# Performance work log

Measured on AMD Instinct MI355X. Metric: run time of the kernel, lower is better.

## Reference

```python
import jax, jax.numpy as jnp
import numpy as np

N_NODES = 100000


def _graph_conv(x, W, b, src, dst, norm):
    # DGL GraphConv(norm='left'): scale source features by 1/out_degree,
    # aggregate (sum over incoming edges). in_feats > out_feats so weight
    # multiply happens before aggregation (mathematically equivalent either way).
    h = x @ W  # [N, out]
    msg = (h * norm[:, None])[src]  # gather per-edge messages [E, out]
    agg = jax.ops.segment_sum(msg, dst, num_segments=N_NODES)
    return agg + b


def setup_inputs() -> dict:
    key = jax.random.key(0)
    ks = jax.random.split(key, 10)
    in_f, hid_f, out_f = 256, 128, 64
    n_edges = 1_600_000
    feat = jax.random.normal(ks[0], (N_NODES, in_f), dtype=jnp.float32)
    src = jax.random.randint(ks[1], (n_edges,), 0, N_NODES, dtype=jnp.int32)
    dst = jax.random.randint(ks[2], (n_edges,), 0, N_NODES, dtype=jnp.int32)
    noise = jax.random.normal(ks[3], (N_NODES, out_f), dtype=jnp.float32)
    s1 = 1.0 / np.sqrt(in_f)
    s2 = 1.0 / np.sqrt(hid_f)
    W_shared = jax.random.uniform(ks[4], (in_f, hid_f), minval=-s1, maxval=s1, dtype=jnp.float32)
    b_shared = jnp.zeros((hid_f,), jnp.float32)
    W_mu = jax.random.uniform(ks[5], (hid_f, out_f), minval=-s2, maxval=s2, dtype=jnp.float32)
    b_mu = jnp.zeros((out_f,), jnp.float32)
    W_ls = jax.random.uniform(ks[6], (hid_f, out_f), minval=-s2, maxval=s2, dtype=jnp.float32)
    b_ls = jnp.zeros((out_f,), jnp.float32)
    return {"feat": feat, "W_shared": W_shared, "b_shared": b_shared,
            "W_mu": W_mu, "b_mu": b_mu, "W_ls": W_ls, "b_ls": b_ls,
            "noise": noise, "src": src, "dst": dst}


def reference(feat, W_shared, b_shared, W_mu, b_mu, W_ls, b_ls, noise, src, dst):
    # left-norm: 1 / out_degree (clamped to >= 1, as DGL does)
    deg_out = jax.ops.segment_sum(jnp.ones_like(src, jnp.float32), src,
                                  num_segments=N_NODES)
    norm = 1.0 / jnp.maximum(deg_out, 1.0)
    # shared first GraphConv with ReLU activation
    h = jax.nn.relu(_graph_conv(feat, W_shared, b_shared, src, dst, norm))
    # two heads (no activation)
    mu = _graph_conv(h, W_mu, b_mu, src, dst, norm)
    log_sigma = _graph_conv(h, W_ls, b_ls, src, dst, norm)
    # reparameterized sample
    return mu + noise * jnp.exp(log_sigma)
```

## Files before the change

### kernel.cpp

```cpp
#include <hip/hip_runtime.h>
#include <hip/hip_bf16.h>
#include <math.h>

typedef __attribute__((ext_vector_type(8))) short short8;
typedef __attribute__((ext_vector_type(4))) float f32x4;

__device__ __forceinline__ unsigned short f2bf(float f) {
    unsigned int u = __float_as_uint(f);
    u += 0x7FFF + ((u >> 16) & 1);
    return (unsigned short)(u >> 16);
}
__device__ __forceinline__ float b2f(unsigned short s) {
    return __uint_as_float(((unsigned int)s) << 16);
}
__device__ __forceinline__ unsigned int f2bf2(float a, float b) {
    __hip_bfloat162 h = __float22bfloat162_rn(make_float2(a, b));
    return *(unsigned int*)&h;
}
__device__ __forceinline__ void gl_lds16(const void* g, void* l) {
    __builtin_amdgcn_global_load_lds(
        (const __attribute__((address_space(1))) void*)g,
        (__attribute__((address_space(3))) void*)l, 16, 0, 0);
}

#define EB 8192
#define BSH 10
#define NBKT 128

__global__ __launch_bounds__(256)
void k1_hist(const int* __restrict__ src, const int* __restrict__ dst,
             int* __restrict__ bhist, int E) {
    __shared__ int hist[256];
    int t = threadIdx.x;
    hist[t] = 0;
    __syncthreads();
    int base = blockIdx.x * EB;
    int end = min(base + EB, E);
    for (int e = base + 4 * t; e < end; e += 1024) {
        if (e + 3 < end) {
            int4 d4 = *(const int4*)&dst[e];
            int4 s4 = *(const int4*)&src[e];
            atomicAdd(&hist[d4.x >> BSH], 1);
            atomicAdd(&hist[d4.y >> BSH], 1);
            atomicAdd(&hist[d4.z >> BSH], 1);
            atomicAdd(&hist[d4.w >> BSH], 1);
            atomicAdd(&hist[128 + (s4.x >> BSH)], 1);
            atomicAdd(&hist[128 + (s4.y >> BSH)], 1);
            atomicAdd(&hist[128 + (s4.z >> BSH)], 1);
            atomicAdd(&hist[128 + (s4.w >> BSH)], 1);
        } else {
            for (int q = e; q < end; ++q) {
                atomicAdd(&hist[dst[q] >> BSH], 1);
                atomicAdd(&hist[128 + (src[q] >> BSH)], 1);
            }
        }
    }
    __syncthreads();
    bhist[(size_t)blockIdx.x * 256 + t] = hist[t];
}

__global__ __launch_bounds__(256)
void kc1_totals(const int* __restrict__ bhist, int* __restrict__ totals, int PB) {
    int t = threadIdx.x;
    int slice = (PB + 7) / 8;
    int b0 = blockIdx.x * slice;
    int b1 = min(b0 + slice, PB);
    int s = 0;
    for (int blk = b0; blk < b1; ++blk) s += bhist[(size_t)blk * 256 + t];
    if (s) atomicAdd(&totals[t], s);
}

__global__ __launch_bounds__(256)
void kc2_scan2(const int* __restrict__ totals, int* __restrict__ bbase_d,
               int* __restrict__ bbase_s) {
    __shared__ int s[256];
    int t = threadIdx.x;
    int v = totals[t];
    s[t] = v;
    __syncthreads();
    for (int off = 1; off < 128; off <<= 1) {
        int u = ((t & 127) >= off) ? s[t - off] : 0;
        __syncthreads();
        s[t] += u;
        __syncthreads();
    }
    int excl = s[t] - v;
    if (t < 128) bbase_d[t] = excl;
    else bbase_s[t - 128] = excl;
}

__global__ __launch_bounds__(256)
void kc3_boff(const int* __restrict__ bhist, const int* __restrict__ bbase_d,
              const int* __restrict__ bbase_s, int* __restrict__ boffT, int PB) {
    __shared__ int sums[256];
    int b = blockIdx.x;
    int t = threadIdx.x;
    int v = (t < PB) ? bhist[(size_t)t * 256 + b] : 0;
    sums[t] = v;
    __syncthreads();
    for (int off = 1; off < 256; off <<= 1) {
        int u = (t >= off) ? sums[t - off] : 0;
        __syncthreads();
        sums[t] += u;
        __syncthreads();
    }
    int base = (b < 128) ? bbase_d[b] : bbase_s[b - 128];
    if (t < PB) boffT[(size_t)b * PB + t] = base + sums[t] - v;
}

__global__ __launch_bounds__(256)
void k2_scatter(const int* __restrict__ src, const int* __restrict__ dst,
                const int* __restrict__ boffT, int2* __restrict__ parr,
                int* __restrict__ sarr, int E, int PB) {
    __shared__ int cnt[256];
    int t = threadIdx.x;
    int blk = blockIdx.x;
    cnt[t] = boffT[(size_t)t * PB + blk];
    __syncthreads();
    int base = blk * EB;
    int end = min(base + EB, E);
    for (int e = base + 4 * t; e < end; e += 1024) {
        if (e + 3 < end) {
            int4 s4 = *(const int4*)&src[e];
            int4 d4 = *(const int4*)&dst[e];
            int p0 = atomicAdd(&cnt[d4.x >> BSH], 1); parr[p0] = make_int2(s4.x, d4.x);
            int p1 = atomicAdd(&cnt[d4.y >> BSH], 1); parr[p1] = make_int2(s4.y, d4.y);
            int p2 = atomicAdd(&cnt[d4.z >> BSH], 1); parr[p2] = make_int2(s4.z, d4.z);
            int p3 = atomicAdd(&cnt[d4.w >> BSH], 1); parr[p3] = make_int2(s4.w, d4.w);
            int q0 = atomicAdd(&cnt[128 + (s4.x >> BSH)], 1); sarr[q0] = s4.x;
            int q1 = atomicAdd(&cnt[128 + (s4.y >> BSH)], 1); sarr[q1] = s4.y;
            int q2 = atomicAdd(&cnt[128 + (s4.z >> BSH)], 1); sarr[q2] = s4.z;
            int q3 = atomicAdd(&cnt[128 + (s4.w >> BSH)], 1); sarr[q3] = s4.w;
        } else {
            for (int q = e; q < end; ++q) {
                int sv = src[q], dv = dst[q];
                int pd = atomicAdd(&cnt[dv >> BSH], 1);
                parr[pd] = make_int2(sv, dv);
                int ps = atomicAdd(&cnt[128 + (sv >> BSH)], 1);
                sarr[ps] = sv;
            }
        }
    }
}

__global__ __launch_bounds__(1024)
void k3_dst(const int2* __restrict__ parr, const int* __restrict__ totals,
            const int* __restrict__ bbase_d, int* __restrict__ row_off,
            int* __restrict__ col, int N, int E) {
    __shared__ int hist[1024], sc[1024];
    int b = blockIdx.x, t = threadIdx.x;
    if (b == 0 && t == 0) row_off[N] = E;
    int ne = totals[b];
    int ebase = bbase_d[b];
    hist[t] = 0;
    __syncthreads();
    for (int i = t; i < ne; i += 1024)
        atomicAdd(&hist[parr[ebase + i].y & 1023], 1);
    __syncthreads();
    int h = hist[t];
    sc[t] = h;
    __syncthreads();
    for (int off = 1; off < 1024; off <<= 1) {
        int u = (t >= off) ? sc[t - off] : 0;
        __syncthreads();
        sc[t] += u;
        __syncthreads();
    }
    int excl = sc[t] - h;
    int node = b * 1024 + t;
    if (node < N) row_off[node] = ebase + excl;
    hist[t] = ebase + excl;
    __syncthreads();
    for (int i = t; i < ne; i += 1024) {
        int2 pr = parr[ebase + i];
        int slot = atomicAdd(&hist[pr.y & 1023], 1);
        col[slot] = pr.x;
    }
}

__global__ __launch_bounds__(1024)
void k3_src(const int* __restrict__ sarr, const int* __restrict__ totals_s,
            const int* __restrict__ bbase_s, float* __restrict__ norm, int N) {
    __shared__ int hist[1024];
    int b = blockIdx.x, t = threadIdx.x;
    int ne = totals_s[b];
    int sb = bbase_s[b];
    hist[t] = 0;
    __syncthreads();
    for (int i = t; i < ne; i += 1024)
        atomicAdd(&hist[sarr[sb + i] & 1023], 1);
    __syncthreads();
    int node = b * 1024 + t;
    if (node < N) {
        int d = hist[t];
        norm[node] = 1.0f / (float)(d > 1 ? d : 1);
    }
}

__global__ __launch_bounds__(256)
void k_wprep(const float* __restrict__ Wsh, const float* __restrict__ Wmu,
             const float* __restrict__ Wls, unsigned short* __restrict__ W1T,
             unsigned short* __restrict__ W2T) {
    int b = blockIdx.x, t = threadIdx.x;
    if (b < 128) {
        W1T[(size_t)b * 256 + t] = f2bf(Wsh[(size_t)t * 128 + b]);
    } else {
        int n = b - 128;
        if (t < 128) {
            float v = (n < 64) ? Wmu[(size_t)t * 64 + n]
                               : Wls[(size_t)t * 64 + (n - 64)];
            W2T[(size_t)n * 128 + t] = f2bf(v);
        }
    }
}

__global__ __launch_bounds__(256)
void k_gemm1(const float* __restrict__ A, int M,
             const unsigned short* __restrict__ W1T,
             const float* __restrict__ norm, unsigned short* __restrict__ outb) {
    __shared__ char ldsA[64 * 1040];
    const int w = threadIdx.x >> 6;
    const int lane = threadIdx.x & 63;
    const int quad = lane >> 4;
    const int l16 = lane & 15;
    const int cl = w * 16 + l16;
    const int r0 = blockIdx.x * 64;

#pragma unroll
    for (int i = 0; i < 16; ++i) {
        int row = r0 + w * 16 + i;
        if (row >= M) row = M - 1;
        const char* g = (const char*)A + (size_t)row * 1024 + lane * 16;
        char* l = ldsA + (w * 16 + i) * 1040 + lane * 16;
        gl_lds16(g, l);
    }

    short8 bw[2][8];
#pragma unroll
    for (int hf = 0; hf < 2; ++hf) {
        const unsigned short* wp = W1T + (size_t)(hf * 64 + cl) * 256 + quad * 8;
#pragma unroll
        for (int ks = 0; ks < 8; ++ks)
            bw[hf][ks] = *(const short8*)(wp + ks * 32);
    }
    __syncthreads();

    f32x4 acc[4][2];
#pragma unroll
    for (int m = 0; m < 4; ++m) {
        acc[m][0] = (f32x4){0.f, 0.f, 0.f, 0.f};
        acc[m][1] = (f32x4){0.f, 0.f, 0.f, 0.f};
    }
#pragma unroll
    for (int ks = 0; ks < 8; ++ks) {
#pragma unroll
        for (int m = 0; m < 4; ++m) {
            const float* pr = (const float*)(ldsA + (m * 16 + l16) * 1040 +
                                             (ks * 32 + quad * 8) * 4);
            float4 x = *(const float4*)pr;
            float4 y = *(const float4*)(pr + 4);
            union { short8 v; unsigned int u[4]; } c;
            c.u[0] = f2bf2(x.x, x.y);
            c.u[1] = f2bf2(x.z, x.w);
            c.u[2] = f2bf2(y.x, y.y);
            c.u[3] = f2bf2(y.z, y.w);
            acc[m][0] = __builtin_amdgcn_mfma_f32_16x16x32_bf16(bw[0][ks], c.v, acc[m][0], 0, 0, 0);
            acc[m][1] = __builtin_amdgcn_mfma_f32_16x16x32_bf16(bw[1][ks], c.v, acc[m][1], 0, 0, 0);
        }
    }
    const int colbase = w * 16 + quad * 4;
#pragma unroll
    for (int m = 0; m < 4; ++m) {
        int row = r0 + m * 16 + l16;
        if (row < M) {
            float nm = norm[row];
            ushort4 o0, o1;
            o0.x = f2bf(acc[m][0][0] * nm); o0.y = f2bf(acc[m][0][1] * nm);
            o0.z = f2bf(acc[m][0][2] * nm); o0.w = f2bf(acc[m][0][3] * nm);
            o1.x = f2bf(acc[m][1][0] * nm); o1.y = f2bf(acc[m][1][1] * nm);
            o1.z = f2bf(acc[m][1][2] * nm); o1.w = f2bf(acc[m][1][3] * nm);
            *(ushort4*)&outb[(size_t)row * 128 + colbase] = o0;
            *(ushort4*)&outb[(size_t)row * 128 + 64 + colbase] = o1;
        }
    }
}

__global__ __launch_bounds__(256)
void k_gemm2(const unsigned short* __restrict__ A, int M,
             const unsigned short* __restrict__ W2T,
             const float* __restrict__ norm, unsigned short* __restrict__ outb) {
    __shared__ char ldsB[16 * 1040];
    const int w = threadIdx.x >> 6;
    const int lane = threadIdx.x & 63;
    const int quad = lane >> 4;
    const int l16 = lane & 15;
    const int cl = w * 16 + l16;
    const int r0 = blockIdx.x * 64;

#pragma unroll
    for (int i = 0; i < 4; ++i) {
        int c = w * 4 + i;
        int crow = r0 + c * 4;
        if (crow + 4 > M) crow = M - 4;
        const char* g = (const char*)A + (size_t)crow * 256 + lane * 16;
        char* l = ldsB + c * 1040 + lane * 16;
        gl_lds16(g, l);
    }

    short8 bw[2][4];
#pragma unroll
    for (int hf = 0; hf < 2; ++hf) {
        const unsigned short* wp = W2T + (size_t)(hf * 64 + cl) * 128 + quad * 8;
#pragma unroll
        for (int ks = 0; ks < 4; ++ks)
            bw[hf][ks] = *(const short8*)(wp + ks * 32);
    }
    __syncthreads();

    f32x4 acc[4][2];
#pragma unroll
    for (int m = 0; m < 4; ++m) {
        acc[m][0] = (f32x4){0.f, 0.f, 0.f, 0.f};
        acc[m][1] = (f32x4){0.f, 0.f, 0.f, 0.f};
    }
#pragma unroll
    for (int ks = 0; ks < 4; ++ks) {
#pragma unroll
        for (int m = 0; m < 4; ++m) {
            int row = m * 16 + l16;
            short8 af = *(const short8*)(ldsB + (row >> 2) * 1040 + (row & 3) * 256 +
                                         (ks * 32 + quad * 8) * 2);
            acc[m][0] = __builtin_amdgcn_mfma_f32_16x16x32_bf16(bw[0][ks], af, acc[m][0], 0, 0, 0);
            acc[m][1] = __builtin_amdgcn_mfma_f32_16x16x32_bf16(bw[1][ks], af, acc[m][1], 0, 0, 0);
        }
    }
    const int colbase = w * 16 + quad * 4;
#pragma unroll
    for (int m = 0; m < 4; ++m) {
        int row = r0 + m * 16 + l16;
        if (row < M) {
            float nm = norm[row];
            ushort4 o0, o1;
            o0.x = f2bf(acc[m][0][0] * nm); o0.y = f2bf(acc[m][0][1] * nm);
            o0.z = f2bf(acc[m][0][2] * nm); o0.w = f2bf(acc[m][0][3] * nm);
            o1.x = f2bf(acc[m][1][0] * nm); o1.y = f2bf(acc[m][1][1] * nm);
            o1.z = f2bf(acc[m][1][2] * nm); o1.w = f2bf(acc[m][1][3] * nm);
            *(ushort4*)&outb[(size_t)row * 128 + colbase] = o0;
            *(ushort4*)&outb[(size_t)row * 128 + 64 + colbase] = o1;
        }
    }
}

__global__ __launch_bounds__(256)
void k_spmm_relu(const int* __restrict__ row_off, const int* __restrict__ col,
                 const unsigned short* __restrict__ hxb, const float* __restrict__ bias,
                 unsigned short* __restrict__ hb, int N) {
    int g = (blockIdx.x * blockDim.x + threadIdx.x) >> 5;
    int l = threadIdx.x & 31;
    if (g >= N) return;
    int e0 = row_off[g], e1 = row_off[g + 1];
    const ushort4* base = (const ushort4*)hxb;
    float4 acc = make_float4(0.f, 0.f, 0.f, 0.f);
    int e = e0;
    for (; e + 7 < e1; e += 8) {
        ushort4 v0 = base[(size_t)col[e] * 32 + l];
        ushort4 v1 = base[(size_t)col[e + 1] * 32 + l];
        ushort4 v2 = base[(size_t)col[e + 2] * 32 + l];
        ushort4 v3 = base[(size_t)col[e + 3] * 32 + l];
        ushort4 v4 = base[(size_t)col[e + 4] * 32 + l];
        ushort4 v5 = base[(size_t)col[e + 5] * 32 + l];
        ushort4 v6 = base[(size_t)col[e + 6] * 32 + l];
        ushort4 v7 = base[(size_t)col[e + 7] * 32 + l];
        acc.x += ((b2f(v0.x) + b2f(v1.x)) + (b2f(v2.x) + b2f(v3.x))) +
                 ((b2f(v4.x) + b2f(v5.x)) + (b2f(v6.x) + b2f(v7.x)));
        acc.y += ((b2f(v0.y) + b2f(v1.y)) + (b2f(v2.y) + b2f(v3.y))) +
                 ((b2f(v4.y) + b2f(v5.y)) + (b2f(v6.y) + b2f(v7.y)));
        acc.z += ((b2f(v0.z) + b2f(v1.z)) + (b2f(v2.z) + b2f(v3.z))) +
                 ((b2f(v4.z) + b2f(v5.z)) + (b2f(v6.z) + b2f(v7.z)));
        acc.w += ((b2f(v0.w) + b2f(v1.w)) + (b2f(v2.w) + b2f(v3.w))) +
                 ((b2f(v4.w) + b2f(v5.w)) + (b2f(v6.w) + b2f(v7.w)));
    }
    for (; e + 1 < e1; e += 2) {
        ushort4 a = base[(size_t)col[e] * 32 + l];
        ushort4 b = base[(size_t)col[e + 1] * 32 + l];
        acc.x += b2f(a.x) + b2f(b.x);
        acc.y += b2f(a.y) + b2f(b.y);
        acc.z += b2f(a.z) + b2f(b.z);
        acc.w += b2f(a.w) + b2f(b.w);
    }
    if (e < e1) {
        ushort4 a = base[(size_t)col[e] * 32 + l];
        acc.x += b2f(a.x); acc.y += b2f(a.y); acc.z += b2f(a.z); acc.w += b2f(a.w);
    }
    float4 bi = ((const float4*)bias)[l];
    ushort4 r;
    r.x = f2bf(fmaxf(acc.x + bi.x, 0.f));
    r.y = f2bf(fmaxf(acc.y + bi.y, 0.f));
    r.z = f2bf(fmaxf(acc.z + bi.z, 0.f));
    r.w = f2bf(fmaxf(acc.w + bi.w, 0.f));
    ((ushort4*)hb)[(size_t)g * 32 + l] = r;
}

__global__ __launch_bounds__(256)
void k_spmm_out(const int* __restrict__ row_off, const int* __restrict__ col,
                const unsigned short* __restrict__ hcb, const float* __restrict__ bmu,
                const float* __restrict__ bls, const float* __restrict__ noise,
                float* __restrict__ out, int N) {
    int g = (blockIdx.x * blockDim.x + threadIdx.x) >> 5;
    int l = threadIdx.x & 31;
    if (g >= N) return;
    int e0 = row_off[g], e1 = row_off[g + 1];
    const ushort4* base = (const ushort4*)hcb;
    float4 acc = make_float4(0.f, 0.f, 0.f, 0.f);
    int e = e0;
    for (; e + 7 < e1; e += 8) {
        ushort4 v0 = base[(size_t)col[e] * 32 + l];
        ushort4 v1 = base[(size_t)col[e + 1] * 32 + l];
        ushort4 v2 = base[(size_t)col[e + 2] * 32 + l];
        ushort4 v3 = base[(size_t)col[e + 3] * 32 + l];
        ushort4 v4 = base[(size_t)col[e + 4] * 32 + l];
        ushort4 v5 = base[(size_t)col[e + 5] * 32 + l];
        ushort4 v6 = base[(size_t)col[e + 6] * 32 + l];
        ushort4 v7 = base[(size_t)col[e + 7] * 32 + l];
        acc.x += ((b2f(v0.x) + b2f(v1.x)) + (b2f(v2.x) + b2f(v3.x))) +
                 ((b2f(v4.x) + b2f(v5.x)) + (b2f(v6.x) + b2f(v7.x)));
        acc.y += ((b2f(v0.y) + b2f(v1.y)) + (b2f(v2.y) + b2f(v3.y))) +
                 ((b2f(v4.y) + b2f(v5.y)) + (b2f(v6.y) + b2f(v7.y)));
        acc.z += ((b2f(v0.z) + b2f(v1.z)) + (b2f(v2.z) + b2f(v3.z))) +
                 ((b2f(v4.z) + b2f(v5.z)) + (b2f(v6.z) + b2f(v7.z)));
        acc.w += ((b2f(v0.w) + b2f(v1.w)) + (b2f(v2.w) + b2f(v3.w))) +
                 ((b2f(v4.w) + b2f(v5.w)) + (b2f(v6.w) + b2f(v7.w)));
    }
    for (; e + 1 < e1; e += 2) {
        ushort4 a = base[(size_t)col[e] * 32 + l];
        ushort4 b = base[(size_t)col[e + 1] * 32 + l];
        acc.x += b2f(a.x) + b2f(b.x);
        acc.y += b2f(a.y) + b2f(b.y);
        acc.z += b2f(a.z) + b2f(b.z);
        acc.w += b2f(a.w) + b2f(b.w);
    }
    if (e < e1) {
        ushort4 a = base[(size_t)col[e] * 32 + l];
        acc.x += b2f(a.x); acc.y += b2f(a.y); acc.z += b2f(a.z); acc.w += b2f(a.w);
    }
    int lane64 = threadIdx.x & 63;
    int p = (lane64 + 16) & 63;
    float lx = __shfl(acc.x, p, 64);
    float ly = __shfl(acc.y, p, 64);
    float lz = __shfl(acc.z, p, 64);
    float lw = __shfl(acc.w, p, 64);
    if (l < 16) {
        float4 bm = ((const float4*)bmu)[l];
        float4 bl = ((const float4*)bls)[l];
        float4 nz = ((const float4*)noise)[(size_t)g * 16 + l];
        float4 o;
        o.x = (acc.x + bm.x) + nz.x * expf(lx + bl.x);
        o.y = (acc.y + bm.y) + nz.y * expf(ly + bl.y);
        o.z = (acc.z + bm.z) + nz.z * expf(lz + bl.z);
        o.w = (acc.w + bm.w) + nz.w * expf(lw + bl.w);
        ((float4*)out)[(size_t)g * 16 + l] = o;
    }
}

static inline char* align64(char* p) {
    return (char*)(((uintptr_t)p + 63) & ~(uintptr_t)63);
}

extern "C" void kernel_launch(void* const* d_in, const int* in_sizes, int n_in,
                              void* d_out, int out_size, void* d_ws, size_t ws_size,
                              hipStream_t stream) {
    const float* feat  = (const float*)d_in[0];
    const float* Wsh   = (const float*)d_in[1];
    const float* bsh   = (const float*)d_in[2];
    const float* Wmu   = (const float*)d_in[3];
    const float* bmu   = (const float*)d_in[4];
    const float* Wls   = (const float*)d_in[5];
    const float* bls   = (const float*)d_in[6];
    const float* noise = (const float*)d_in[7];
    const int*   src   = (const int*)d_in[8];
    const int*   dst   = (const int*)d_in[9];
    float* out = (float*)d_out;

    const int N = in_sizes[0] / 256;
    const int E = in_sizes[8];
    const int PB = (E + EB - 1) / EB;

    char* p = (char*)d_ws;
    float* norm   = (float*)p;                  p += (size_t)N * 4;         p = align64(p);
    int* row_off  = (int*)p;                    p += (size_t)(N + 4) * 4;   p = align64(p);
    int* totals   = (int*)p;                    p += 256 * 4;
    int* bbase_d  = (int*)p;                    p += 128 * 4;
    int* bbase_s  = (int*)p;                    p += 128 * 4;               p = align64(p);
    unsigned short* W1T = (unsigned short*)p;   p += (size_t)128 * 256 * 2;
    unsigned short* W2T = (unsigned short*)p;   p += (size_t)128 * 128 * 2;
    p = align64(p);
    int* bhist    = (int*)p;                    p += (size_t)PB * 256 * 4;  p = align64(p);
    int* boffT    = (int*)p;                    p += (size_t)256 * PB * 4;  p = align64(p);
    int2* parr    = (int2*)p;                   p += (size_t)E * 8;
    int* sarr     = (int*)p;                    p += (size_t)E * 4;
    int* col      = (int*)p;                    p += (size_t)E * 4;         p = align64(p);
    unsigned short* hxb = (unsigned short*)p;
    unsigned short* hb  = (unsigned short*)d_out;

    hipMemsetAsync(totals, 0, 256 * sizeof(int), stream);
    k_wprep<<<256, 256, 0, stream>>>(Wsh, Wmu, Wls, W1T, W2T);
    k1_hist<<<PB, 256, 0, stream>>>(src, dst, bhist, E);
    kc1_totals<<<8, 256, 0, stream>>>(bhist, totals, PB);
    kc2_scan2<<<1, 256, 0, stream>>>(totals, bbase_d, bbase_s);
    kc3_boff<<<256, 256, 0, stream>>>(bhist, bbase_d, bbase_s, boffT, PB);
    k2_scatter<<<PB, 256, 0, stream>>>(src, dst, boffT, parr, sarr, E, PB);
    k3_dst<<<NBKT, 1024, 0, stream>>>(parr, totals, bbase_d, row_off, col, N, E);
    k3_src<<<NBKT, 1024, 0, stream>>>(sarr, totals + 128, bbase_s, norm, N);

    int gtiles = (N + 63) / 64;
    k_gemm1<<<gtiles, 256, 0, stream>>>(feat, N, W1T, norm, hxb);
    k_spmm_relu<<<(N * 32 + 255) / 256, 256, 0, stream>>>(row_off, col, hxb, bsh, hb, N);
    k_gemm2<<<gtiles, 256, 0, stream>>>(hb, N, W2T, norm, hxb);
    k_spmm_out<<<(N * 32 + 255) / 256, 256, 0, stream>>>(row_off, col, hxb, bmu, bls, noise, out, N);
}
```

Measured before the change: 449.8 us.

## Build CSR with global degree atomics and scan instead of two-level bucket sort

Replaces the two-pass bucketed radix-style CSR construction (histogram, bucket offsets, scatter to intermediate pairs, per-bucket local sort) with direct global-atomic degree counting, a three-kernel prefix scan, and an atomic scatter of source ids into col. This removes the intermediate parr/sarr buffers and several small kernels. In exchange it relies on heavily contended global atomics across 100k nodes, and edges within a row now land in nondeterministic order, which can change floating-point summation order and hurt locality of the gathers.

Measured after the change: 624.6 us. +38.9%, slower.

```diff
diff --git a/kernel.cpp b/kernel.cpp
--- a/kernel.cpp
+++ b/kernel.cpp
@@ -23,142 +23,37 @@
         (__attribute__((address_space(3))) void*)l, 16, 0, 0);
 }
 
-#define EB 8192
-#define BSH 10
-#define NBKT 128
-
-__global__ __launch_bounds__(256)
-void k1_hist(const int* __restrict__ src, const int* __restrict__ dst,
-             int* __restrict__ bhist, int E) {
-    __shared__ int hist[256];
-    int t = threadIdx.x;
-    hist[t] = 0;
-    __syncthreads();
-    int base = blockIdx.x * EB;
-    int end = min(base + EB, E);
-    for (int e = base + 4 * t; e < end; e += 1024) {
-        if (e + 3 < end) {
-            int4 d4 = *(const int4*)&dst[e];
-            int4 s4 = *(const int4*)&src[e];
-            atomicAdd(&hist[d4.x >> BSH], 1);
-            atomicAdd(&hist[d4.y >> BSH], 1);
-            atomicAdd(&hist[d4.z >> BSH], 1);
-            atomicAdd(&hist[d4.w >> BSH], 1);
-            atomicAdd(&hist[128 + (s4.x >> BSH)], 1);
-            atomicAdd(&hist[128 + (s4.y >> BSH)], 1);
-            atomicAdd(&hist[128 + (s4.z >> BSH)], 1);
-            atomicAdd(&hist[128 + (s4.w >> BSH)], 1);
-        } else {
-            for (int q = e; q < end; ++q) {
-                atomicAdd(&hist[dst[q] >> BSH], 1);
-                atomicAdd(&hist[128 + (src[q] >> BSH)], 1);
-            }
-        }
-    }
-    __syncthreads();
-    bhist[(size_t)blockIdx.x * 256 + t] = hist[t];
-}
-
-__global__ __launch_bounds__(256)
-void kc1_totals(const int* __restrict__ bhist, int* __restrict__ totals, int PB) {
-    int t = threadIdx.x;
-    int slice = (PB + 7) / 8;
-    int b0 = blockIdx.x * slice;
-    int b1 = min(b0 + slice, PB);
-    int s = 0;
-    for (int blk = b0; blk < b1; ++blk) s += bhist[(size_t)blk * 256 + t];
-    if (s) atomicAdd(&totals[t], s);
-}
-
-__global__ __launch_bounds__(256)
-void kc2_scan2(const int* __restrict__ totals, int* __restrict__ bbase_d,
-               int* __restrict__ bbase_s) {
-    __shared__ int s[256];
-    int t = threadIdx.x;
-    int v = totals[t];
-    s[t] = v;
-    __syncthreads();
-    for (int off = 1; off < 128; off <<= 1) {
-        int u = ((t & 127) >= off) ? s[t - off] : 0;
-        __syncthreads();
-        s[t] += u;
-        __syncthreads();
-    }
-    int excl = s[t] - v;
-    if (t < 128) bbase_d[t] = excl;
-    else bbase_s[t - 128] = excl;
-}
-
-__global__ __launch_bounds__(256)
-void kc3_boff(const int* __restrict__ bhist, const int* __restrict__ bbase_d,
-              const int* __restrict__ bbase_s, int* __restrict__ boffT, int PB) {
-    __shared__ int sums[256];
-    int b = blockIdx.x;
-    int t = threadIdx.x;
-    int v = (t < PB) ? bhist[(size_t)t * 256 + b] : 0;
-    sums[t] = v;
-    __syncthreads();
-    for (int off = 1; off < 256; off <<= 1) {
-        int u = (t >= off) ? sums[t - off] : 0;
-        __syncthreads();
-        sums[t] += u;
-        __syncthreads();
-    }
-    int base = (b < 128) ? bbase_d[b] : bbase_s[b - 128];
-    if (t < PB) boffT[(size_t)b * PB + t] = base + sums[t] - v;
-}
-
-__global__ __launch_bounds__(256)
-void k2_scatter(const int* __restrict__ src, const int* __restrict__ dst,
-                const int* __restrict__ boffT, int2* __restrict__ parr,
-                int* __restrict__ sarr, int E, int PB) {
-    __shared__ int cnt[256];
-    int t = threadIdx.x;
-    int blk = blockIdx.x;
-    cnt[t] = boffT[(size_t)t * PB + blk];
-    __syncthreads();
-    int base = blk * EB;
-    int end = min(base + EB, E);
-    for (int e = base + 4 * t; e < end; e += 1024) {
-        if (e + 3 < end) {
-            int4 s4 = *(const int4*)&src[e];
-            int4 d4 = *(const int4*)&dst[e];
-            int p0 = atomicAdd(&cnt[d4.x >> BSH], 1); parr[p0] = make_int2(s4.x, d4.x);
-            int p1 = atomicAdd(&cnt[d4.y >> BSH], 1); parr[p1] = make_int2(s4.y, d4.y);
-            int p2 = atomicAdd(&cnt[d4.z >> BSH], 1); parr[p2] = make_int2(s4.z, d4.z);
-            int p3 = atomicAdd(&cnt[d4.w >> BSH], 1); parr[p3] = make_int2(s4.w, d4.w);
-            int q0 = atomicAdd(&cnt[128 + (s4.x >> BSH)], 1); sarr[q0] = s4.x;
-            int q1 = atomicAdd(&cnt[128 + (s4.y >> BSH)], 1); sarr[q1] = s4.y;
-            int q2 = atomicAdd(&cnt[128 + (s4.z >> BSH)], 1); sarr[q2] = s4.z;
-            int q3 = atomicAdd(&cnt[128 + (s4.w >> BSH)], 1); sarr[q3] = s4.w;
-        } else {
-            for (int q = e; q < end; ++q) {
-                int sv = src[q], dv = dst[q];
-                int pd = atomicAdd(&cnt[dv >> BSH], 1);
-                parr[pd] = make_int2(sv, dv);
-                int ps = atomicAdd(&cnt[128 + (sv >> BSH)], 1);
-                sarr[ps] = sv;
-            }
-        }
+
+__global__ __launch_bounds__(256)
+void k_deg(const int* __restrict__ src, const int* __restrict__ dst,
+           int* __restrict__ degS, int* __restrict__ degD, int E) {
+    int t = blockIdx.x * 256 + threadIdx.x;
+    int n4 = E >> 2;
+    if (t < n4) {
+        int4 s4 = ((const int4*)src)[t];
+        int4 d4 = ((const int4*)dst)[t];
+        atomicAdd(&degS[s4.x], 1); atomicAdd(&degS[s4.y], 1);
+        atomicAdd(&degS[s4.z], 1); atomicAdd(&degS[s4.w], 1);
+        atomicAdd(&degD[d4.x], 1); atomicAdd(&degD[d4.y], 1);
+        atomicAdd(&degD[d4.z], 1); atomicAdd(&degD[d4.w], 1);
+    }
+    int rem = E & 3;
+    if (t < rem) {
+        int e = (n4 << 2) + t;
+        atomicAdd(&degS[src[e]], 1);
+        atomicAdd(&degD[dst[e]], 1);
     }
 }
 
 __global__ __launch_bounds__(1024)
-void k3_dst(const int2* __restrict__ parr, const int* __restrict__ totals,
-            const int* __restrict__ bbase_d, int* __restrict__ row_off,
-            int* __restrict__ col, int N, int E) {
-    __shared__ int hist[1024], sc[1024];
+void kscan_a(const int* __restrict__ degD, const int* __restrict__ degS,
+             int* __restrict__ row_off, float* __restrict__ norm,
+             int* __restrict__ btot, int N) {
+    __shared__ int sc[1024];
     int b = blockIdx.x, t = threadIdx.x;
-    if (b == 0 && t == 0) row_off[N] = E;
-    int ne = totals[b];
-    int ebase = bbase_d[b];
-    hist[t] = 0;
-    __syncthreads();
-    for (int i = t; i < ne; i += 1024)
-        atomicAdd(&hist[parr[ebase + i].y & 1023], 1);
-    __syncthreads();
-    int h = hist[t];
-    sc[t] = h;
+    int i = b * 1024 + t;
+    int v = (i < N) ? degD[i] : 0;
+    sc[t] = v;
     __syncthreads();
     for (int off = 1; off < 1024; off <<= 1) {
         int u = (t >= off) ? sc[t - off] : 0;
@@ -166,36 +61,64 @@
         sc[t] += u;
         __syncthreads();
     }
-    int excl = sc[t] - h;
-    int node = b * 1024 + t;
-    if (node < N) row_off[node] = ebase + excl;
-    hist[t] = ebase + excl;
+    if (i < N) {
+        row_off[i] = sc[t] - v;
+        int ds = degS[i];
+        norm[i] = 1.0f / (float)(ds > 1 ? ds : 1);
+    }
+    if (t == 1023) btot[b] = sc[t];
+}
+
+__global__ __launch_bounds__(128)
+void kscan_b(const int* __restrict__ btot, int* __restrict__ bbase,
+             int* __restrict__ row_off, int NB, int N, int E) {
+    __shared__ int sc[128];
+    int t = threadIdx.x;
+    int v = (t < NB) ? btot[t] : 0;
+    sc[t] = v;
     __syncthreads();
-    for (int i = t; i < ne; i += 1024) {
-        int2 pr = parr[ebase + i];
-        int slot = atomicAdd(&hist[pr.y & 1023], 1);
-        col[slot] = pr.x;
-    }
+    for (int off = 1; off < 128; off <<= 1) {
+        int u = (t >= off) ? sc[t - off] : 0;
+        __syncthreads();
+        sc[t] += u;
+        __syncthreads();
+    }
+    if (t < NB) bbase[t] = sc[t] - v;
+    if (t == 0) row_off[N] = E;
 }
 
 __global__ __launch_bounds__(1024)
-void k3_src(const int* __restrict__ sarr, const int* __restrict__ totals_s,
-            const int* __restrict__ bbase_s, float* __restrict__ norm, int N) {
-    __shared__ int hist[1024];
-    int b = blockIdx.x, t = threadIdx.x;
-    int ne = totals_s[b];
-    int sb = bbase_s[b];
-    hist[t] = 0;
-    __syncthreads();
-    for (int i = t; i < ne; i += 1024)
-        atomicAdd(&hist[sarr[sb + i] & 1023], 1);
-    __syncthreads();
-    int node = b * 1024 + t;
-    if (node < N) {
-        int d = hist[t];
-        norm[node] = 1.0f / (float)(d > 1 ? d : 1);
-    }
-}
+void kscan_c(int* __restrict__ row_off, const int* __restrict__ bbase,
+             int* __restrict__ pos, int N) {
+    int i = blockIdx.x * 1024 + threadIdx.x;
+    if (i < N) {
+        int r = row_off[i] + bbase[blockIdx.x];
+        row_off[i] = r;
+        pos[i] = r;
+    }
+}
+
+__global__ __launch_bounds__(256)
+void k_scatter2(const int* __restrict__ src, const int* __restrict__ dst,
+                int* __restrict__ pos, int* __restrict__ col, int E) {
+    int t = blockIdx.x * 256 + threadIdx.x;
+    int n4 = E >> 2;
+    if (t < n4) {
+        int4 s4 = ((const int4*)src)[t];
+        int4 d4 = ((const int4*)dst)[t];
+        int p0 = atomicAdd(&pos[d4.x], 1); col[p0] = s4.x;
+        int p1 = atomicAdd(&pos[d4.y], 1); col[p1] = s4.y;
+        int p2 = atomicAdd(&pos[d4.z], 1); col[p2] = s4.z;
+        int p3 = atomicAdd(&pos[d4.w], 1); col[p3] = s4.w;
+    }
+    int rem = E & 3;
+    if (t < rem) {
+        int e = (n4 << 2) + t;
+        int p = atomicAdd(&pos[dst[e]], 1);
+        col[p] = src[e];
+    }
+}
+
 
 __global__ __launch_bounds__(256)
 void k_wprep(const float* __restrict__ Wsh, const float* __restrict__ Wmu,
@@ -483,38 +406,37 @@
 
     const int N = in_sizes[0] / 256;
     const int E = in_sizes[8];
-    const int PB = (E + EB - 1) / EB;
+    const int NB = (N + 1023) >> 10;
 
     char* p = (char*)d_ws;
     float* norm   = (float*)p;                  p += (size_t)N * 4;         p = align64(p);
     int* row_off  = (int*)p;                    p += (size_t)(N + 4) * 4;   p = align64(p);
-    int* totals   = (int*)p;                    p += 256 * 4;
-    int* bbase_d  = (int*)p;                    p += 128 * 4;
-    int* bbase_s  = (int*)p;                    p += 128 * 4;               p = align64(p);
+    int* degS     = (int*)p;                    p += (size_t)N * 4;
+    int* degD     = (int*)p;                    p += (size_t)N * 4;
+    p = align64(p);
+    int* pos      = (int*)p;                    p += (size_t)N * 4;         p = align64(p);
+    int* btot     = (int*)p;                    p += 128 * 4;
+    int* bbase    = (int*)p;                    p += 128 * 4;               p = align64(p);
     unsigned short* W1T = (unsigned short*)p;   p += (size_t)128 * 256 * 2;
     unsigned short* W2T = (unsigned short*)p;   p += (size_t)128 * 128 * 2;
     p = align64(p);
-    int* bhist    = (int*)p;                    p += (size_t)PB * 256 * 4;  p = align64(p);
-    int* boffT    = (int*)p;                    p += (size_t)256 * PB * 4;  p = align64(p);
-    int2* parr    = (int2*)p;                   p += (size_t)E * 8;
-    int* sarr     = (int*)p;                    p += (size_t)E * 4;
     int* col      = (int*)p;                    p += (size_t)E * 4;         p = align64(p);
     unsigned short* hxb = (unsigned short*)p;
     unsigned short* hb  = (unsigned short*)d_out;
 
-    hipMemsetAsync(totals, 0, 256 * sizeof(int), stream);
+    const int gE = ((E >> 2) + 255) / 256;
+
+    hipMemsetAsync(degS, 0, (size_t)2 * N * sizeof(int), stream);
     k_wprep<<<256, 256, 0, stream>>>(Wsh, Wmu, Wls, W1T, W2T);
-    k1_hist<<<PB, 256, 0, stream>>>(src, dst, bhist, E);
-    kc1_totals<<<8, 256, 0, stream>>>(bhist, totals, PB);
-    kc2_scan2<<<1, 256, 0, stream>>>(totals, bbase_d, bbase_s);
-    kc3_boff<<<256, 256, 0, stream>>>(bhist, bbase_d, bbase_s, boffT, PB);
-    k2_scatter<<<PB, 256, 0, stream>>>(src, dst, boffT, parr, sarr, E, PB);
-    k3_dst<<<NBKT, 1024, 0, stream>>>(parr, totals, bbase_d, row_off, col, N, E);
-    k3_src<<<NBKT, 1024, 0, stream>>>(sarr, totals + 128, bbase_s, norm, N);
+    k_deg<<<gE, 256, 0, stream>>>(src, dst, degS, degD, E);
+    kscan_a<<<NB, 1024, 0, stream>>>(degD, degS, row_off, norm, btot, N);
+    kscan_b<<<1, 128, 0, stream>>>(btot, bbase, row_off, NB, N, E);
+    kscan_c<<<NB, 1024, 0, stream>>>(row_off, bbase, pos, N);
+    k_scatter2<<<gE, 256, 0, stream>>>(src, dst, pos, col, E);
 
     int gtiles = (N + 63) / 64;
     k_gemm1<<<gtiles, 256, 0, stream>>>(feat, N, W1T, norm, hxb);
     k_spmm_relu<<<(N * 32 + 255) / 256, 256, 0, stream>>>(row_off, col, hxb, bsh, hb, N);
-    k_gemm2<<<gtiles, 256, 0, stream>>>(hb, N, W2T, norm, hxb);
+    k_gemm2<<<gtiles, 256, 0, stream>>>(hb, W2T ? N : N, W2T, norm, hxb);
     k_spmm_out<<<(N * 32 + 255) / 256, 256, 0, stream>>>(row_off, col, hxb, bmu, bls, noise, out, N);
 }
```

## Compute out-degree with global atomics and pack edge pairs into one int

Applied to the files above, without the earlier changes.

Source out-degrees are now counted with global atomics into a per-node array inside the histogram kernel. This removes the source-bucket scatter array, its bucket histogram and the k3_src pass, and a small kernel turns the counts into norm. The dst-bucketed edge records are packed as (src<<10 | dst&1023) in one int instead of an int2, halving scatter traffic. The cost is 1.6M scattered global atomics, and the packing assumes src fits in 22 bits.

Result: slower. 486.9 us (+8.2%).

```diff
diff --git a/kernel.cpp b/kernel.cpp
--- a/kernel.cpp
+++ b/kernel.cpp
@@ -29,10 +29,10 @@
 
 __global__ __launch_bounds__(256)
 void k1_hist(const int* __restrict__ src, const int* __restrict__ dst,
-             int* __restrict__ bhist, int E) {
-    __shared__ int hist[256];
+             int* __restrict__ bhist, int* __restrict__ degS, int E) {
+    __shared__ int hist[NBKT];
     int t = threadIdx.x;
-    hist[t] = 0;
+    if (t < NBKT) hist[t] = 0;
     __syncthreads();
     int base = blockIdx.x * EB;
     int end = min(base + EB, E);
@@ -44,58 +44,55 @@
             atomicAdd(&hist[d4.y >> BSH], 1);
             atomicAdd(&hist[d4.z >> BSH], 1);
             atomicAdd(&hist[d4.w >> BSH], 1);
-            atomicAdd(&hist[128 + (s4.x >> BSH)], 1);
-            atomicAdd(&hist[128 + (s4.y >> BSH)], 1);
-            atomicAdd(&hist[128 + (s4.z >> BSH)], 1);
-            atomicAdd(&hist[128 + (s4.w >> BSH)], 1);
+            atomicAdd(&degS[s4.x], 1);
+            atomicAdd(&degS[s4.y], 1);
+            atomicAdd(&degS[s4.z], 1);
+            atomicAdd(&degS[s4.w], 1);
         } else {
             for (int q = e; q < end; ++q) {
                 atomicAdd(&hist[dst[q] >> BSH], 1);
-                atomicAdd(&hist[128 + (src[q] >> BSH)], 1);
+                atomicAdd(&degS[src[q]], 1);
             }
         }
     }
     __syncthreads();
-    bhist[(size_t)blockIdx.x * 256 + t] = hist[t];
-}
-
-__global__ __launch_bounds__(256)
+    if (t < NBKT) bhist[(size_t)blockIdx.x * NBKT + t] = hist[t];
+}
+
+__global__ __launch_bounds__(128)
 void kc1_totals(const int* __restrict__ bhist, int* __restrict__ totals, int PB) {
     int t = threadIdx.x;
     int slice = (PB + 7) / 8;
     int b0 = blockIdx.x * slice;
     int b1 = min(b0 + slice, PB);
     int s = 0;
-    for (int blk = b0; blk < b1; ++blk) s += bhist[(size_t)blk * 256 + t];
+    for (int blk = b0; blk < b1; ++blk) s += bhist[(size_t)blk * NBKT + t];
     if (s) atomicAdd(&totals[t], s);
 }
 
-__global__ __launch_bounds__(256)
-void kc2_scan2(const int* __restrict__ totals, int* __restrict__ bbase_d,
-               int* __restrict__ bbase_s) {
-    __shared__ int s[256];
+__global__ __launch_bounds__(128)
+void kc2_scan(const int* __restrict__ totals, int* __restrict__ bbase_d) {
+    __shared__ int s[128];
     int t = threadIdx.x;
     int v = totals[t];
     s[t] = v;
     __syncthreads();
     for (int off = 1; off < 128; off <<= 1) {
-        int u = ((t & 127) >= off) ? s[t - off] : 0;
+        int u = (t >= off) ? s[t - off] : 0;
         __syncthreads();
         s[t] += u;
         __syncthreads();
     }
-    int excl = s[t] - v;
-    if (t < 128) bbase_d[t] = excl;
-    else bbase_s[t - 128] = excl;
+    bbase_d[t] = s[t] - v;
 }
 
 __global__ __launch_bounds__(256)
 void kc3_boff(const int* __restrict__ bhist, const int* __restrict__ bbase_d,
-              const int* __restrict__ bbase_s, int* __restrict__ boffT, int PB) {
+              int* __restrict__ boffT, int PB) {
     __shared__ int sums[256];
     int b = blockIdx.x;
     int t = threadIdx.x;
-    int v = (t < PB) ? bhist[(size_t)t * 256 + b] : 0;
+    int v = (t < PB) ? bhist[(size_t)t * NBKT + b] : 0;
     sums[t] = v;
     __syncthreads();
     for (int off = 1; off < 256; off <<= 1) {
@@ -104,18 +101,26 @@
         sums[t] += u;
         __syncthreads();
     }
-    int base = (b < 128) ? bbase_d[b] : bbase_s[b - 128];
-    if (t < PB) boffT[(size_t)b * PB + t] = base + sums[t] - v;
+    if (t < PB) boffT[(size_t)b * PB + t] = bbase_d[b] + sums[t] - v;
+}
+
+__global__ __launch_bounds__(256)
+void k_norm(const int* __restrict__ degS, float* __restrict__ norm, int N) {
+    int i = blockIdx.x * 256 + threadIdx.x;
+    if (i < N) {
+        int d = degS[i];
+        norm[i] = 1.0f / (float)(d > 1 ? d : 1);
+    }
 }
 
 __global__ __launch_bounds__(256)
 void k2_scatter(const int* __restrict__ src, const int* __restrict__ dst,
-                const int* __restrict__ boffT, int2* __restrict__ parr,
-                int* __restrict__ sarr, int E, int PB) {
-    __shared__ int cnt[256];
+                const int* __restrict__ boffT, int* __restrict__ parr,
+                int E, int PB) {
+    __shared__ int cnt[NBKT];
     int t = threadIdx.x;
     int blk = blockIdx.x;
-    cnt[t] = boffT[(size_t)t * PB + blk];
+    if (t < NBKT) cnt[t] = boffT[(size_t)t * PB + blk];
     __syncthreads();
     int base = blk * EB;
     int end = min(base + EB, E);
@@ -123,28 +128,26 @@
         if (e + 3 < end) {
             int4 s4 = *(const int4*)&src[e];
             int4 d4 = *(const int4*)&dst[e];
-            int p0 = atomicAdd(&cnt[d4.x >> BSH], 1); parr[p0] = make_int2(s4.x, d4.x);
-            int p1 = atomicAdd(&cnt[d4.y >> BSH], 1); parr[p1] = make_int2(s4.y, d4.y);
-            int p2 = atomicAdd(&cnt[d4.z >> BSH], 1); parr[p2] = make_int2(s4.z, d4.z);
-            int p3 = atomicAdd(&cnt[d4.w >> BSH], 1); parr[p3] = make_int2(s4.w, d4.w);
-            int q0 = atomicAdd(&cnt[128 + (s4.x >> BSH)], 1); sarr[q0] = s4.x;
-            int q1 = atomicAdd(&cnt[128 + (s4.y >> BSH)], 1); sarr[q1] = s4.y;
-            int q2 = atomicAdd(&cnt[128 + (s4.z >> BSH)], 1); sarr[q2] = s4.z;
-            int q3 = atomicAdd(&cnt[128 + (s4.w >> BSH)], 1); sarr[q3] = s4.w;
+            int p0 = atomicAdd(&cnt[d4.x >> BSH], 1);
+            parr[p0] = (s4.x << BSH) | (d4.x & (1024 - 1));
+            int p1 = atomicAdd(&cnt[d4.y >> BSH], 1);
+            parr[p1] = (s4.y << BSH) | (d4.y & (1024 - 1));
+            int p2 = atomicAdd(&cnt[d4.z >> BSH], 1);
+            parr[p2] = (s4.z << BSH) | (d4.z & (1024 - 1));
+            int p3 = atomicAdd(&cnt[d4.w >> BSH], 1);
+            parr[p3] = (s4.w << BSH) | (d4.w & (1024 - 1));
         } else {
             for (int q = e; q < end; ++q) {
                 int sv = src[q], dv = dst[q];
                 int pd = atomicAdd(&cnt[dv >> BSH], 1);
-                parr[pd] = make_int2(sv, dv);
-                int ps = atomicAdd(&cnt[128 + (sv >> BSH)], 1);
-                sarr[ps] = sv;
+                parr[pd] = (sv << BSH) | (dv & (1024 - 1));
             }
         }
     }
 }
 
 __global__ __launch_bounds__(1024)
-void k3_dst(const int2* __restrict__ parr, const int* __restrict__ totals,
+void k3_dst(const int* __restrict__ parr, const int* __restrict__ totals,
             const int* __restrict__ bbase_d, int* __restrict__ row_off,
             int* __restrict__ col, int N, int E) {
     __shared__ int hist[1024], sc[1024];
@@ -155,7 +158,7 @@
     hist[t] = 0;
     __syncthreads();
     for (int i = t; i < ne; i += 1024)
-        atomicAdd(&hist[parr[ebase + i].y & 1023], 1);
+        atomicAdd(&hist[parr[ebase + i] & 1023], 1);
     __syncthreads();
     int h = hist[t];
     sc[t] = h;
@@ -172,30 +175,12 @@
     hist[t] = ebase + excl;
     __syncthreads();
     for (int i = t; i < ne; i += 1024) {
-        int2 pr = parr[ebase + i];
-        int slot = atomicAdd(&hist[pr.y & 1023], 1);
-        col[slot] = pr.x;
-    }
-}
-
-__global__ __launch_bounds__(1024)
-void k3_src(const int* __restrict__ sarr, const int* __restrict__ totals_s,
-            const int* __restrict__ bbase_s, float* __restrict__ norm, int N) {
-    __shared__ int hist[1024];
-    int b = blockIdx.x, t = threadIdx.x;
-    int ne = totals_s[b];
-    int sb = bbase_s[b];
-    hist[t] = 0;
-    __syncthreads();
-    for (int i = t; i < ne; i += 1024)
-        atomicAdd(&hist[sarr[sb + i] & 1023], 1);
-    __syncthreads();
-    int node = b * 1024 + t;
-    if (node < N) {
-        int d = hist[t];
-        norm[node] = 1.0f / (float)(d > 1 ? d : 1);
-    }
-}
+        int pr = parr[ebase + i];
+        int slot = atomicAdd(&hist[pr & 1023], 1);
+        col[slot] = pr >> BSH;
+    }
+}
+
 
 __global__ __launch_bounds__(256)
 void k_wprep(const float* __restrict__ Wsh, const float* __restrict__ Wmu,
@@ -488,29 +473,28 @@
     char* p = (char*)d_ws;
     float* norm   = (float*)p;                  p += (size_t)N * 4;         p = align64(p);
     int* row_off  = (int*)p;                    p += (size_t)(N + 4) * 4;   p = align64(p);
-    int* totals   = (int*)p;                    p += 256 * 4;
-    int* bbase_d  = (int*)p;                    p += 128 * 4;
-    int* bbase_s  = (int*)p;                    p += 128 * 4;               p = align64(p);
+    int* degS     = (int*)p;                    p += (size_t)N * 4;
+    int* totals   = (int*)p;                    p += 128 * 4;
+    int* bbase_d  = (int*)p;                    p += 128 * 4;               p = align64(p);
     unsigned short* W1T = (unsigned short*)p;   p += (size_t)128 * 256 * 2;
     unsigned short* W2T = (unsigned short*)p;   p += (size_t)128 * 128 * 2;
     p = align64(p);
-    int* bhist    = (int*)p;                    p += (size_t)PB * 256 * 4;  p = align64(p);
-    int* boffT    = (int*)p;                    p += (size_t)256 * PB * 4;  p = align64(p);
-    int2* parr    = (int2*)p;                   p += (size_t)E * 8;
-    int* sarr     = (int*)p;                    p += (size_t)E * 4;
+    int* bhist    = (int*)p;                    p += (size_t)PB * NBKT * 4; p = align64(p);
+    int* boffT    = (int*)p;                    p += (size_t)NBKT * PB * 4; p = align64(p);
+    int* parr     = (int*)p;                    p += (size_t)E * 4;
     int* col      = (int*)p;                    p += (size_t)E * 4;         p = align64(p);
     unsigned short* hxb = (unsigned short*)p;
     unsigned short* hb  = (unsigned short*)d_out;
 
-    hipMemsetAsync(totals, 0, 256 * sizeof(int), stream);
+    hipMemsetAsync(degS, 0, (size_t)N * 4 + 128 * 4, stream);
     k_wprep<<<256, 256, 0, stream>>>(Wsh, Wmu, Wls, W1T, W2T);
-    k1_hist<<<PB, 256, 0, stream>>>(src, dst, bhist, E);
-    kc1_totals<<<8, 256, 0, stream>>>(bhist, totals, PB);
-    kc2_scan2<<<1, 256, 0, stream>>>(totals, bbase_d, bbase_s);
-    kc3_boff<<<256, 256, 0, stream>>>(bhist, bbase_d, bbase_s, boffT, PB);
-    k2_scatter<<<PB, 256, 0, stream>>>(src, dst, boffT, parr, sarr, E, PB);
+    k1_hist<<<PB, 256, 0, stream>>>(src, dst, bhist, degS, E);
+    kc1_totals<<<8, 128, 0, stream>>>(bhist, totals, PB);
+    kc2_scan<<<1, 128, 0, stream>>>(totals, bbase_d);
+    kc3_boff<<<NBKT, 256, 0, stream>>>(bhist, bbase_d, boffT, PB);
+    k_norm<<<(N + 255) / 256, 256, 0, stream>>>(degS, norm, N);
+    k2_scatter<<<PB, 256, 0, stream>>>(src, dst, boffT, parr, E, PB);
     k3_dst<<<NBKT, 1024, 0, stream>>>(parr, totals, bbase_d, row_off, col, N, E);
-    k3_src<<<NBKT, 1024, 0, stream>>>(sarr, totals + 128, bbase_s, norm, N);
 
     int gtiles = (N + 63) / 64;
     k_gemm1<<<gtiles, 256, 0, stream>>>(feat, N, W1T, norm, hxb);
```
